# Optimization experiments

Hardware: AMD Instinct MI355X
Metric: run time of the kernel (lower is better)

The kernel has to match this reference:

```python
import jax, jax.numpy as jnp
import numpy as np

B, S, H = 4, 2048, 1024
D_FF = 4 * H
NUM_EXPERTS = 8
TOP_K = 2


def setup_inputs() -> dict:
    key = jax.random.key(0)
    ks = jax.random.split(key, 6)
    scale = 0.02
    return {
        "hidden_states": jax.random.normal(ks[0], (B, S, H), dtype=jnp.float32),
        "w_router": jax.random.normal(ks[1], (NUM_EXPERTS, H), dtype=jnp.float32) * scale,
        "w1": jax.random.normal(ks[2], (NUM_EXPERTS, D_FF, H), dtype=jnp.float32) * scale,
        "b1": jnp.zeros((NUM_EXPERTS, D_FF), dtype=jnp.float32),
        "w2": jax.random.normal(ks[3], (NUM_EXPERTS, H, D_FF), dtype=jnp.float32) * scale,
        "b2": jnp.zeros((NUM_EXPERTS, H), dtype=jnp.float32),
    }


def reference(hidden_states, w_router, w1, b1, w2, b2):
    Bc, Sc, Hc = hidden_states.shape
    E = w_router.shape[0]
    dtype = hidden_states.dtype

    # Router: logits [B, S, E], top-k, softmax over the k selected logits.
    router_logits = jnp.einsum("bsh,eh->bse", hidden_states, w_router)
    topk_values, topk_indices = jax.lax.top_k(router_logits, TOP_K)
    topk_weights = jax.nn.softmax(topk_values.astype(jnp.float32), axis=-1).astype(dtype)

    # Per-token combine weight for each expert: [B, S, E] -> [T, E].
    # (Equivalent to the torch sort/group + weighted index_add_ combine.)
    combine = jnp.sum(
        jax.nn.one_hot(topk_indices, E, dtype=dtype) * topk_weights[..., None], axis=-2
    )
    flat = hidden_states.reshape(-1, Hc)          # [T, H]
    cw = combine.reshape(-1, E)                    # [T, E]

    # Dense-equivalent MoE: each expert MLP runs on all tokens, scaled by its
    # combine weight (zero for unrouted tokens) -> identical math to gather/scatter.
    mixed = jnp.zeros_like(flat)
    for e in range(E):
        h1 = jax.nn.gelu(flat @ w1[e].T + b1[e], approximate=False)  # [T, 4H]
        mixed = mixed + cw[:, e:e + 1] * (h1 @ w2[e].T + b2[e])
    return mixed.reshape(Bc, Sc, Hc)
```

## Files before the change

kernel.cpp:

```cpp
#include <hip/hip_runtime.h>
#include <hip/hip_bf16.h>
#include <math.h>


#define TT  8192
#define HD  1024
#define DFF 4096
#define NE  8
#define ROWCAP 17408
#define MAXTILES 136

typedef __attribute__((ext_vector_type(8))) short short8;
typedef __attribute__((ext_vector_type(4))) float f32x4;

static __device__ __forceinline__ unsigned short f2bf(float f) {
    unsigned int u = __float_as_uint(f);
    unsigned int r = (u + 0x7fffu + ((u >> 16) & 1u)) >> 16;
    return (unsigned short)r;
}

static __device__ __forceinline__ void gload_lds16(const void* gp, void* lp) {
    __builtin_amdgcn_global_load_lds(
        (__attribute__((address_space(1))) void*)(void*)gp,
        (__attribute__((address_space(3))) void*)lp,
        16, 0, 0);
}

__global__ __launch_bounds__(256) void cvt_w_kernel(const float* __restrict__ s,
                                                    unsigned short* __restrict__ d) {
    const long i = (long)blockIdx.x * 256 + threadIdx.x;
    float4 v = ((const float4*)s)[i];
    ushort4 o;
    o.x = f2bf(v.x); o.y = f2bf(v.y); o.z = f2bf(v.z); o.w = f2bf(v.w);
    ((ushort4*)d)[i] = o;
}

__global__ __launch_bounds__(256) void router_kernel(const float* __restrict__ x,
                                                     const float* __restrict__ wr,
                                                     int* __restrict__ tokE,
                                                     float* __restrict__ tokW,
                                                     int* __restrict__ counts) {
    const int token = blockIdx.x * 4 + (threadIdx.x >> 6);
    const int lane = threadIdx.x & 63;
    const float* xp = x + (long)token * HD;
    double lg[NE];
#pragma unroll
    for (int e = 0; e < NE; ++e) {
        const float* wp = wr + e * HD;
        double s = 0.0;
        for (int i = lane; i < HD; i += 64) s += (double)xp[i] * (double)wp[i];
#pragma unroll
        for (int off = 32; off > 0; off >>= 1) s += __shfl_xor(s, off, 64);
        lg[e] = s;
    }
    if (lane == 0) {
        int i0 = 0; double v0 = lg[0];
#pragma unroll
        for (int e = 1; e < NE; ++e) if (lg[e] > v0) { v0 = lg[e]; i0 = e; }
        int i1 = -1; double v1 = -1e300;
#pragma unroll
        for (int e = 0; e < NE; ++e) if (e != i0 && lg[e] > v1) { v1 = lg[e]; i1 = e; }
        double p = exp(v1 - v0);
        double d = 1.0 + p;
        tokE[token * 2] = i0;     tokW[token * 2] = (float)(1.0 / d);
        tokE[token * 2 + 1] = i1; tokW[token * 2 + 1] = (float)(p / d);
        atomicAdd(&counts[i0], 1);
        atomicAdd(&counts[i1], 1);
    }
}

__global__ void setup_kernel(const int* __restrict__ counts,
                             int* __restrict__ cursor,
                             int* __restrict__ tileExpert,
                             int* __restrict__ tileRow0) {
    if (threadIdx.x == 0 && blockIdx.x == 0) {
        int off = 0, t = 0;
        for (int e = 0; e < NE; ++e) {
            cursor[e] = off;
            const int padded = (counts[e] + 127) & ~127;
            for (int i = 0; i < padded / 128; ++i) {
                tileExpert[t] = e;
                tileRow0[t] = off + i * 128;
                ++t;
            }
            off += padded;
        }
        for (; t < MAXTILES; ++t) tileExpert[t] = -1;
    }
}

__global__ __launch_bounds__(256) void init_rows_kernel(int* __restrict__ rowTok,
                                                        float* __restrict__ rowCw) {
    const int i = blockIdx.x * 256 + threadIdx.x;
    rowTok[i] = 0;
    rowCw[i] = 0.f;
}

__global__ __launch_bounds__(256) void scatter_kernel(const int* __restrict__ tokE,
                                                      const float* __restrict__ tokW,
                                                      int* __restrict__ cursor,
                                                      int* __restrict__ rowTok,
                                                      float* __restrict__ rowCw) {
    const int t = blockIdx.x * 256 + threadIdx.x;
#pragma unroll
    for (int j = 0; j < 2; ++j) {
        const int e = tokE[t * 2 + j];
        const int pos = atomicAdd(&cursor[e], 1);
        rowTok[pos] = t;
        rowCw[pos] = tokW[t * 2 + j];
    }
}

__global__ __launch_bounds__(256) void gather_kernel(const float* __restrict__ x,
                                                     const int* __restrict__ rowTok,
                                                     unsigned short* __restrict__ Xg) {
    const int row = blockIdx.x;
    const int tok = rowTok[row];
    const float4 v = ((const float4*)(x + (long)tok * HD))[threadIdx.x];
    ushort4 o;
    o.x = f2bf(v.x); o.y = f2bf(v.y); o.z = f2bf(v.z); o.w = f2bf(v.w);
    ((ushort4*)(Xg + (long)row * HD))[threadIdx.x] = o;
}

template <int EPI, int N, int K>
__global__ __launch_bounds__(256) void gemm_moe(
    const unsigned short* __restrict__ A,
    const unsigned short* __restrict__ W,
    const int* __restrict__ tileExpert,
    const int* __restrict__ tileRow0,
    unsigned short* __restrict__ Hout,
    const float* __restrict__ bias,
    float* __restrict__ Out,
    const float* __restrict__ rowCw,
    const int* __restrict__ rowTok) {
    const int e = tileExpert[blockIdx.x];
    if (e < 0) return;

    __shared__ unsigned short As[128 * 32];
    __shared__ unsigned short Bs[128 * 32];

    const int tid = threadIdx.x;
    const int lane = tid & 63;
    const int quad = lane >> 4;
    const int l15 = lane & 15;
    const int wy = (tid >> 6) >> 1;
    const int wx = (tid >> 6) & 1;
    const long row0 = tileRow0[blockIdx.x];
    const long n0 = (long)blockIdx.y * 128;
    const unsigned short* Ab = A + row0 * K;
    const unsigned short* Bb = W + ((long)e * N + n0) * K;

    f32x4 acc[4][4];
#pragma unroll
    for (int i = 0; i < 4; ++i)
#pragma unroll
        for (int j = 0; j < 4; ++j) acc[i][j] = (f32x4){0.f, 0.f, 0.f, 0.f};

    for (int k0 = 0; k0 < K; k0 += 32) {
#pragma unroll
        for (int it = 0; it < 2; ++it) {
            const int c = it * 256 + tid;
            gload_lds16(Ab + (long)(c >> 2) * K + k0 + (c & 3) * 8, As + c * 8);
            gload_lds16(Bb + (long)(c >> 2) * K + k0 + (c & 3) * 8, Bs + c * 8);
        }
        __syncthreads();

        short8 af[4];
#pragma unroll
        for (int mi = 0; mi < 4; ++mi)
            af[mi] = *(const short8*)(As + (wy * 64 + mi * 16 + l15) * 32 + quad * 8);
#pragma unroll
        for (int ni = 0; ni < 4; ++ni) {
            const short8 bf = *(const short8*)(Bs + (wx * 64 + ni * 16 + l15) * 32 + quad * 8);
#pragma unroll
            for (int mi = 0; mi < 4; ++mi)
                acc[mi][ni] = __builtin_amdgcn_mfma_f32_16x16x32_bf16(
                    af[mi], bf, acc[mi][ni], 0, 0, 0);
        }
        __syncthreads();
    }

#pragma unroll
    for (int mi = 0; mi < 4; ++mi) {
        const int lrow0 = wy * 64 + mi * 16 + quad * 4;
#pragma unroll
        for (int ni = 0; ni < 4; ++ni) {
            const long col = n0 + wx * 64 + ni * 16 + l15;
            const float bcol = bias[(long)e * N + col];
#pragma unroll
            for (int r = 0; r < 4; ++r) {
                const long grow = row0 + lrow0 + r;
                const float v = acc[mi][ni][r] + bcol;
                if constexpr (EPI == 0) {
                    const float g = 0.5f * v * (1.0f + erff(v * 0.70710678f));
                    Hout[grow * N + col] = f2bf(g);
                } else {
                    const float w = rowCw[grow];
                    if (w != 0.f)
                        atomicAdd(&Out[(long)rowTok[grow] * HD + col], w * v);
                }
            }
        }
    }
}

extern "C" void kernel_launch(void* const* d_in, const int* in_sizes, int n_in,
                              void* d_out, int out_size, void* d_ws, size_t ws_size,
                              hipStream_t stream) {
    const float* x  = (const float*)d_in[0];
    const float* wr = (const float*)d_in[1];
    const float* w1 = (const float*)d_in[2];
    const float* b1 = (const float*)d_in[3];
    const float* w2 = (const float*)d_in[4];
    const float* b2 = (const float*)d_in[5];
    float* out = (float*)d_out;

    char* p = (char*)d_ws;
    auto alloc = [&](size_t bytes) {
        char* r = p;
        p += (bytes + 255) & ~(size_t)255;
        return r;
    };
    unsigned short* Xg  = (unsigned short*)alloc((size_t)ROWCAP * HD * 2);
    unsigned short* H1g = (unsigned short*)alloc((size_t)ROWCAP * DFF * 2);
    unsigned short* Wb  = (unsigned short*)alloc((size_t)NE * DFF * HD * 2);
    float* rowCw   = (float*)alloc((size_t)ROWCAP * 4);
    int*   rowTok  = (int*)alloc((size_t)ROWCAP * 4);
    int*   tokE    = (int*)alloc((size_t)TT * 2 * 4);
    float* tokW    = (float*)alloc((size_t)TT * 2 * 4);
    int*   counts  = (int*)alloc(64);
    int*   cursor  = (int*)alloc(64);
    int*   tileExpert = (int*)alloc(MAXTILES * 4);
    int*   tileRow0   = (int*)alloc(MAXTILES * 4);

    hipMemsetAsync(out, 0, sizeof(float) * (size_t)TT * HD, stream);
    hipMemsetAsync(counts, 0, 64, stream);

    router_kernel<<<dim3(TT / 4), dim3(256), 0, stream>>>(x, wr, tokE, tokW, counts);
    setup_kernel<<<dim3(1), dim3(64), 0, stream>>>(counts, cursor, tileExpert, tileRow0);
    init_rows_kernel<<<dim3(ROWCAP / 256), dim3(256), 0, stream>>>(rowTok, rowCw);
    scatter_kernel<<<dim3(TT / 256), dim3(256), 0, stream>>>(tokE, tokW, cursor, rowTok, rowCw);
    gather_kernel<<<dim3(ROWCAP), dim3(256), 0, stream>>>(x, rowTok, Xg);

    cvt_w_kernel<<<dim3(NE * DFF * HD / 4 / 256), dim3(256), 0, stream>>>(w1, Wb);
    gemm_moe<0, DFF, HD><<<dim3(MAXTILES, DFF / 128), dim3(256), 0, stream>>>(
        Xg, Wb, tileExpert, tileRow0, H1g, b1, nullptr, nullptr, nullptr);

    cvt_w_kernel<<<dim3(NE * HD * DFF / 4 / 256), dim3(256), 0, stream>>>(w2, Wb);
    gemm_moe<1, HD, DFF><<<dim3(MAXTILES, HD / 128), dim3(256), 0, stream>>>(
        H1g, Wb, tileExpert, tileRow0, nullptr, b2, out, rowCw, rowTok);
}
```

Baseline: 1.192 ms.

## Replace atomic scatter-add combine with bf16 staging and per-token combine kernel

The second GEMM now writes its per-row outputs as bf16 into a staging buffer instead of doing fp32 atomicAdds into the output, and a new combine kernel gathers each token's two expert rows and blends them with the routing weights. This removes the output memset and the atomic traffic. GELU is switched from erf to a tanh-style sigmoid approximation, and the row-init and setup kernels are merged into one launch. In exchange it adds an extra bf16 rounding of the expert outputs and uses an approximate GELU, which slightly changes numerics.

```diff
diff --git a/kernel.cpp b/kernel.cpp
--- a/kernel.cpp
+++ b/kernel.cpp
@@ -17,6 +17,15 @@
     unsigned int u = __float_as_uint(f);
     unsigned int r = (u + 0x7fffu + ((u >> 16) & 1u)) >> 16;
     return (unsigned short)r;
+}
+
+static __device__ __forceinline__ float bf2f(unsigned short u) {
+    return __uint_as_float((unsigned int)u << 16);
+}
+
+static __device__ __forceinline__ float gelu_fast(float v) {
+    const float s = v * (1.5957691f + 0.07135481f * v * v);
+    return v / (1.f + __expf(-s));
 }
 
 static __device__ __forceinline__ void gload_lds16(const void* gp, void* lp) {
@@ -69,18 +78,21 @@
     }
 }
 
-__global__ void setup_kernel(const int* __restrict__ counts,
-                             int* __restrict__ cursor,
-                             int* __restrict__ tileExpert,
-                             int* __restrict__ tileRow0) {
-    if (threadIdx.x == 0 && blockIdx.x == 0) {
+__global__ __launch_bounds__(256) void init_setup_kernel(const int* __restrict__ counts,
+                                                         int* __restrict__ cursor,
+                                                         int* __restrict__ tileExpert,
+                                                         int* __restrict__ tileRow0,
+                                                         int* __restrict__ rowTok) {
+    const int i = blockIdx.x * 256 + threadIdx.x;
+    if (i < ROWCAP) rowTok[i] = 0;
+    if (blockIdx.x == gridDim.x - 1 && threadIdx.x == 0) {
         int off = 0, t = 0;
         for (int e = 0; e < NE; ++e) {
             cursor[e] = off;
             const int padded = (counts[e] + 127) & ~127;
-            for (int i = 0; i < padded / 128; ++i) {
+            for (int j = 0; j < padded / 128; ++j) {
                 tileExpert[t] = e;
-                tileRow0[t] = off + i * 128;
+                tileRow0[t] = off + j * 128;
                 ++t;
             }
             off += padded;
@@ -89,25 +101,17 @@
     }
 }
 
-__global__ __launch_bounds__(256) void init_rows_kernel(int* __restrict__ rowTok,
-                                                        float* __restrict__ rowCw) {
-    const int i = blockIdx.x * 256 + threadIdx.x;
-    rowTok[i] = 0;
-    rowCw[i] = 0.f;
-}
-
 __global__ __launch_bounds__(256) void scatter_kernel(const int* __restrict__ tokE,
-                                                      const float* __restrict__ tokW,
                                                       int* __restrict__ cursor,
                                                       int* __restrict__ rowTok,
-                                                      float* __restrict__ rowCw) {
+                                                      int* __restrict__ posOf) {
     const int t = blockIdx.x * 256 + threadIdx.x;
 #pragma unroll
     for (int j = 0; j < 2; ++j) {
         const int e = tokE[t * 2 + j];
         const int pos = atomicAdd(&cursor[e], 1);
         rowTok[pos] = t;
-        rowCw[pos] = tokW[t * 2 + j];
+        posOf[t * 2 + j] = pos;
     }
 }
 
@@ -129,10 +133,7 @@
     const int* __restrict__ tileExpert,
     const int* __restrict__ tileRow0,
     unsigned short* __restrict__ Hout,
-    const float* __restrict__ bias,
-    float* __restrict__ Out,
-    const float* __restrict__ rowCw,
-    const int* __restrict__ rowTok) {
+    const float* __restrict__ bias) {
     const int e = tileExpert[blockIdx.x];
     if (e < 0) return;
 
@@ -190,18 +191,31 @@
 #pragma unroll
             for (int r = 0; r < 4; ++r) {
                 const long grow = row0 + lrow0 + r;
-                const float v = acc[mi][ni][r] + bcol;
-                if constexpr (EPI == 0) {
-                    const float g = 0.5f * v * (1.0f + erff(v * 0.70710678f));
-                    Hout[grow * N + col] = f2bf(g);
-                } else {
-                    const float w = rowCw[grow];
-                    if (w != 0.f)
-                        atomicAdd(&Out[(long)rowTok[grow] * HD + col], w * v);
-                }
+                float v = acc[mi][ni][r] + bcol;
+                if constexpr (EPI == 0) v = gelu_fast(v);
+                Hout[grow * N + col] = f2bf(v);
             }
         }
     }
+}
+
+__global__ __launch_bounds__(256) void combine_kernel(const unsigned short* __restrict__ Y,
+                                                      const int* __restrict__ posOf,
+                                                      const float* __restrict__ tokW,
+                                                      float* __restrict__ out) {
+    const int t = blockIdx.x;
+    const int p0 = posOf[t * 2];
+    const int p1 = posOf[t * 2 + 1];
+    const float w0 = tokW[t * 2];
+    const float w1 = tokW[t * 2 + 1];
+    const ushort4 a = ((const ushort4*)(Y + (long)p0 * HD))[threadIdx.x];
+    const ushort4 b = ((const ushort4*)(Y + (long)p1 * HD))[threadIdx.x];
+    float4 o;
+    o.x = w0 * bf2f(a.x) + w1 * bf2f(b.x);
+    o.y = w0 * bf2f(a.y) + w1 * bf2f(b.y);
+    o.z = w0 * bf2f(a.z) + w1 * bf2f(b.z);
+    o.w = w0 * bf2f(a.w) + w1 * bf2f(b.w);
+    ((float4*)(out + (long)t * HD))[threadIdx.x] = o;
 }
 
 extern "C" void kernel_launch(void* const* d_in, const int* in_sizes, int n_in,
@@ -224,8 +238,8 @@
     unsigned short* Xg  = (unsigned short*)alloc((size_t)ROWCAP * HD * 2);
     unsigned short* H1g = (unsigned short*)alloc((size_t)ROWCAP * DFF * 2);
     unsigned short* Wb  = (unsigned short*)alloc((size_t)NE * DFF * HD * 2);
-    float* rowCw   = (float*)alloc((size_t)ROWCAP * 4);
     int*   rowTok  = (int*)alloc((size_t)ROWCAP * 4);
+    int*   posOf   = (int*)alloc((size_t)TT * 2 * 4);
     int*   tokE    = (int*)alloc((size_t)TT * 2 * 4);
     float* tokW    = (float*)alloc((size_t)TT * 2 * 4);
     int*   counts  = (int*)alloc(64);
@@ -233,20 +247,23 @@
     int*   tileExpert = (int*)alloc(MAXTILES * 4);
     int*   tileRow0   = (int*)alloc(MAXTILES * 4);
 
-    hipMemsetAsync(out, 0, sizeof(float) * (size_t)TT * HD, stream);
+    unsigned short* Yg = Xg;
+
     hipMemsetAsync(counts, 0, 64, stream);
 
     router_kernel<<<dim3(TT / 4), dim3(256), 0, stream>>>(x, wr, tokE, tokW, counts);
-    setup_kernel<<<dim3(1), dim3(64), 0, stream>>>(counts, cursor, tileExpert, tileRow0);
-    init_rows_kernel<<<dim3(ROWCAP / 256), dim3(256), 0, stream>>>(rowTok, rowCw);
-    scatter_kernel<<<dim3(TT / 256), dim3(256), 0, stream>>>(tokE, tokW, cursor, rowTok, rowCw);
+    init_setup_kernel<<<dim3(ROWCAP / 256 + 1), dim3(256), 0, stream>>>(
+        counts, cursor, tileExpert, tileRow0, rowTok);
+    scatter_kernel<<<dim3(TT / 256), dim3(256), 0, stream>>>(tokE, cursor, rowTok, posOf);
     gather_kernel<<<dim3(ROWCAP), dim3(256), 0, stream>>>(x, rowTok, Xg);
 
     cvt_w_kernel<<<dim3(NE * DFF * HD / 4 / 256), dim3(256), 0, stream>>>(w1, Wb);
     gemm_moe<0, DFF, HD><<<dim3(MAXTILES, DFF / 128), dim3(256), 0, stream>>>(
-        Xg, Wb, tileExpert, tileRow0, H1g, b1, nullptr, nullptr, nullptr);
+        Xg, Wb, tileExpert, tileRow0, H1g, b1);
 
     cvt_w_kernel<<<dim3(NE * HD * DFF / 4 / 256), dim3(256), 0, stream>>>(w2, Wb);
     gemm_moe<1, HD, DFF><<<dim3(MAXTILES, HD / 128), dim3(256), 0, stream>>>(
-        H1g, Wb, tileExpert, tileRow0, nullptr, b2, out, rowCw, rowTok);
-}
+        H1g, Wb, tileExpert, tileRow0, Yg, b2);
+
+    combine_kernel<<<dim3(TT), dim3(256), 0, stream>>>(Yg, posOf, tokW, out);
+}
```

After: 1.091 ms. 1.09x faster.
